# Kernel tuning notes

Measured on AMD Instinct MI355X. Metric: run time of the kernel, lower is better.

## Reference

```python
import jax, jax.numpy as jnp
import numpy as np

C_S, C_Z, C_H = 384, 128, 32
N, L = 4, 384
EPS = 1e-5  # torch LayerNorm default


def setup_inputs() -> dict:
    key = jax.random.key(0)
    ks = jax.random.split(key, 8)
    s = jax.random.normal(ks[0], (N, L, C_S), dtype=jnp.float32)
    ln_g = jnp.ones((C_S,), jnp.float32)
    ln_b = jnp.zeros((C_S,), jnp.float32)
    W1 = jax.random.normal(ks[1], (C_S, C_H), jnp.float32) / np.sqrt(C_S)
    b1 = jax.random.normal(ks[2], (C_H,), jnp.float32) * 0.02
    W2 = jax.random.normal(ks[3], (C_S, C_H), jnp.float32) / np.sqrt(C_S)
    b2 = jax.random.normal(ks[4], (C_H,), jnp.float32) * 0.02
    # linear_out has init='final' (zeros) in training; use random values for a
    # meaningful numerical baseline.
    Wo = jax.random.normal(ks[5], (C_H * C_H, C_Z), jnp.float32) / np.sqrt(C_H * C_H)
    bo = jax.random.normal(ks[6], (C_Z,), jnp.float32) * 0.02
    return {"s": s, "ln_g": ln_g, "ln_b": ln_b, "W1": W1, "b1": b1,
            "W2": W2, "b2": b2, "Wo": Wo, "bo": bo}


def reference(s, ln_g, ln_b, W1, b1, W2, b2, Wo, bo):
    # LayerNorm over c_s
    mu = jnp.mean(s, axis=-1, keepdims=True)
    var = jnp.mean(jnp.square(s - mu), axis=-1, keepdims=True)
    sn = (s - mu) * jax.lax.rsqrt(var + EPS) * ln_g + ln_b
    a = sn @ W1 + b1  # [N, L, c_h]
    b = sn @ W2 + b2  # [N, L, c_h]
    # Original: outer product a[n,i,c]*b[n,j,d] flattened as c*c_h+d, then linear_out.
    # Algebraically fused: never materialize the [N,L,L,c_h^2] tensor.
    Wo3 = Wo.reshape(C_H, C_H, C_Z)  # index order (c, d, z) matches c*c_h+d flattening
    z = jnp.einsum('nic,njd,cdz->nijz', a, b, Wo3, optimize=True) + bo
    return z  # [N, L, L, c_z]
```

## Files before the change

kernel.cpp:

```cpp
#include <hip/hip_runtime.h>
#include <hip/hip_bf16.h>

#define CS 384
#define CH 32
#define CZ 128
#define LL 384
#define NL 1536
#define EPS 1e-5f

typedef float v4f __attribute__((ext_vector_type(4)));
typedef short s8v __attribute__((ext_vector_type(8)));
typedef unsigned short u8s __attribute__((ext_vector_type(8)));

static __device__ __forceinline__ unsigned short f2bf(float x) {
    unsigned int b = __float_as_uint(x);
    b += 0x7FFFu + ((b >> 16) & 1u);
    return (unsigned short)(b >> 16);
}

__global__ __launch_bounds__(256) void k_bf(
    const float* __restrict__ s, const float* __restrict__ g, const float* __restrict__ be,
    const float* __restrict__ W2, const float* __restrict__ pb2,
    unsigned short* __restrict__ BfG)
{
    const int r0 = blockIdx.x * 4;
    const int t  = threadIdx.x;

    __shared__ float sn[4][392];
    __shared__ float part[4][2][32];

    {
        const int w = t >> 6, lane = t & 63;
        const float* srow = s + (size_t)(r0 + w) * CS;
        float x[6];
        #pragma unroll
        for (int k = 0; k < 6; ++k) x[k] = srow[lane + k * 64];
        float p = x[0] + x[1] + x[2] + x[3] + x[4] + x[5];
        #pragma unroll
        for (int m = 1; m < 64; m <<= 1) p += __shfl_xor(p, m);
        const float mu = p * (1.0f / CS);
        float q = 0.f;
        #pragma unroll
        for (int k = 0; k < 6; ++k) { float d = x[k] - mu; q += d * d; }
        #pragma unroll
        for (int m = 1; m < 64; m <<= 1) q += __shfl_xor(q, m);
        const float rstd = rsqrtf(q * (1.0f / CS) + EPS);
        #pragma unroll
        for (int k = 0; k < 6; ++k) {
            const int c = lane + k * 64;
            sn[w][c] = (x[k] - mu) * rstd * g[c] + be[c];
        }
    }
    __syncthreads();

    {
        const int h = t & 31, ch = (t >> 5) & 1, rw = t >> 6;
        const float* snr = sn[rw];
        float acc = 0.f;
        const int c0 = ch * 192;
        #pragma unroll 8
        for (int c = c0; c < c0 + 192; ++c)
            acc += snr[c] * W2[c * CH + h];
        part[rw][ch][h] = acc;
    }
    __syncthreads();

    if (t < 128) {
        const int rw = t >> 5, h = t & 31;
        const float v = part[rw][0][h] + part[rw][1][h] + pb2[h];
        const int row = r0 + rw;
        const int n = row / LL, jr = row % LL;
        const int jt = jr >> 4, l16 = jr & 15;
        BfG[(((size_t)(n * 24 + jt)) * 64 + l16 + 16 * (h >> 3)) * 8 + (h & 7)] = f2bf(v);
    }
}

__global__ __launch_bounds__(256, 3) void k_out_f(
    const float* __restrict__ s, const float* __restrict__ g, const float* __restrict__ be,
    const float* __restrict__ W1, const float* __restrict__ pb1,
    const float* __restrict__ Wo, const unsigned short* __restrict__ BfG,
    const float* __restrict__ bo, float* __restrict__ out)
{
    const int r = blockIdx.x;
    const int t = threadIdx.x;
    const int l = t & 63, w = t >> 6;
    const int g2 = l >> 4, c16 = l & 15;
    const int li = l & 31, hi2 = l >> 5;
    const int n = r / LL;

    __shared__ float sn[392];
    __shared__ float red[8];
    __shared__ float part[8][32];
    __shared__ float Afl[CH];
    __shared__ __align__(16) float Msub[4096];
    __shared__ __align__(16) float bounce[4][2048];

    {
        const float* srow = s + (size_t)r * CS;
        const float e0 = srow[t];
        const float e1 = (t < 128) ? srow[256 + t] : 0.f;
        float p = e0 + e1;
        #pragma unroll
        for (int m = 1; m < 64; m <<= 1) p += __shfl_xor(p, m);
        if (l == 0) red[w] = p;
        __syncthreads();
        const float mu = (red[0] + red[1] + red[2] + red[3]) * (1.0f / CS);
        __syncthreads();
        const float d0 = e0 - mu, d1 = e1 - mu;
        float q = d0 * d0 + ((t < 128) ? d1 * d1 : 0.f);
        #pragma unroll
        for (int m = 1; m < 64; m <<= 1) q += __shfl_xor(q, m);
        if (l == 0) red[w] = q;
        __syncthreads();
        const float var = (red[0] + red[1] + red[2] + red[3]) * (1.0f / CS);
        const float rstd = rsqrtf(var + EPS);
        sn[t] = d0 * rstd * g[t] + be[t];
        if (t < 128) sn[256 + t] = d1 * rstd * g[256 + t] + be[256 + t];
    }
    __syncthreads();

    {
        const int h = t & 31, cs = t >> 5;
        float acc = 0.f;
        const int c0 = cs * 48;
        #pragma unroll 8
        for (int c = c0; c < c0 + 48; ++c)
            acc += sn[c] * W1[c * CH + h];
        part[cs][h] = acc;
    }
    __syncthreads();
    if (t < 32) {
        float a = pb1[t];
        #pragma unroll
        for (int k = 0; k < 8; ++k) a += part[k][t];
        Afl[t] = a;
    }
    __syncthreads();

    {
        const v4f* Wo4 = (const v4f*)Wo;
        #pragma unroll
        for (int it = 0; it < 4; ++it) {
            const int col = t + it * 256;
            v4f acc = (v4f)(0.f);
            #pragma unroll 8
            for (int c = 0; c < CH; ++c)
                acc += Afl[c] * Wo4[(size_t)c * 1024 + col];
            *(v4f*)&Msub[col * 4] = acc;
        }
    }
    __syncthreads();

    s8v mf[8];
    #pragma unroll
    for (int zt = 0; zt < 8; ++zt) {
        u8s o;
        #pragma unroll
        for (int e = 0; e < 8; ++e)
            o[e] = f2bf(Msub[(g2 * 8 + e) * 128 + zt * 16 + c16]);
        mf[zt] = (s8v)o;
    }

    s8v af[6];
    {
        const s8v* Bfn = (const s8v*)(BfG + (size_t)n * 24 * 64 * 8);
        #pragma unroll
        for (int i = 0; i < 6; ++i) af[i] = Bfn[(w + i * 4) * 64 + l];
    }
    v4f bov[8];
    #pragma unroll
    for (int zt = 0; zt < 8; ++zt) bov[zt] = *(const v4f*)(bo + zt * 16 + g2 * 4);

    char* myl = (char*)bounce[w];
    v4f* outv = (v4f*)(out + (size_t)r * LL * CZ);

    #pragma unroll
    for (int i = 0; i < 6; ++i) {
        const int jt = w + i * 4;

        #pragma unroll
        for (int zt = 0; zt < 8; ++zt) {
            v4f d = __builtin_amdgcn_mfma_f32_16x16x32_bf16(mf[zt], af[i], (v4f)(0.f), 0, 0, 0);
            d += bov[zt];
            const int byte = (c16 << 9) + (((zt << 6) + (g2 << 4)) ^ ((c16 & 7) << 4));
            *(v4f*)(myl + byte) = d;
        }
        asm volatile("s_waitcnt lgkmcnt(0)" ::: "memory");

        #pragma unroll
        for (int i2 = 0; i2 < 8; ++i2) {
            const int rw2 = 2 * i2 + hi2;
            const int byte = (rw2 << 9) + (((li << 4)) ^ ((rw2 & 7) << 4));
            const v4f v = *(const v4f*)(myl + byte);
            outv[(size_t)(jt * 16 + rw2) * 32 + li] = v;
        }
    }
}

extern "C" void kernel_launch(void* const* d_in, const int* in_sizes, int n_in,
                              void* d_out, int out_size, void* d_ws, size_t ws_size,
                              hipStream_t stream) {
    const float* s  = (const float*)d_in[0];
    const float* g  = (const float*)d_in[1];
    const float* be = (const float*)d_in[2];
    const float* W1 = (const float*)d_in[3];
    const float* b1 = (const float*)d_in[4];
    const float* W2 = (const float*)d_in[5];
    const float* b2 = (const float*)d_in[6];
    const float* Wo = (const float*)d_in[7];
    const float* bo = (const float*)d_in[8];
    float* out = (float*)d_out;

    if (ws_size < 98304u) return;
    unsigned short* Bf = (unsigned short*)d_ws;

    k_bf   <<<NL / 4, 256, 0, stream>>>(s, g, be, W2, b2, Bf);
    k_out_f<<<NL, 256, 0, stream>>>(s, g, be, W1, b1, Wo, Bf, bo, out);
}
```

Before: 85.55 us.

## Process two rows per block and pre-convert Wo to bf16 once

The first kernel now also converts Wo to bf16 in workspace. The output kernel handles two L rows per block, so each Wo load feeds two A vectors when building the 32x128 M matrices. M is stored directly as transposed bf16 in shared memory, which replaces the strided per-element conversion from fp32. The aim is to halve the per-row Wo traffic and drop redundant conversion work, at the cost of fewer blocks, more shared memory, and an extra barrier between rows.

After: 81.00 us. 1.06x faster.

```diff
diff --git a/kernel.cpp b/kernel.cpp
--- a/kernel.cpp
+++ b/kernel.cpp
@@ -17,14 +17,33 @@
     b += 0x7FFFu + ((b >> 16) & 1u);
     return (unsigned short)(b >> 16);
 }
+static __device__ __forceinline__ v4f bf4_to_f4(ushort4 h) {
+    v4f r;
+    r.x = __uint_as_float((unsigned)h.x << 16);
+    r.y = __uint_as_float((unsigned)h.y << 16);
+    r.z = __uint_as_float((unsigned)h.z << 16);
+    r.w = __uint_as_float((unsigned)h.w << 16);
+    return r;
+}
 
 __global__ __launch_bounds__(256) void k_bf(
     const float* __restrict__ s, const float* __restrict__ g, const float* __restrict__ be,
     const float* __restrict__ W2, const float* __restrict__ pb2,
-    unsigned short* __restrict__ BfG)
+    const float* __restrict__ Wo,
+    unsigned short* __restrict__ BfG, unsigned short* __restrict__ Wob)
 {
     const int r0 = blockIdx.x * 4;
     const int t  = threadIdx.x;
+
+    {
+        const int idx = blockIdx.x * 256 + t;
+        if (idx < (CH * CH * CZ) / 4) {
+            const v4f v = ((const v4f*)Wo)[idx];
+            ushort4 h;
+            h.x = f2bf(v.x); h.y = f2bf(v.y); h.z = f2bf(v.z); h.w = f2bf(v.w);
+            ((ushort4*)Wob)[idx] = h;
+        }
+    }
 
     __shared__ float sn[4][392];
     __shared__ float part[4][2][32];
@@ -78,88 +97,87 @@
 __global__ __launch_bounds__(256, 3) void k_out_f(
     const float* __restrict__ s, const float* __restrict__ g, const float* __restrict__ be,
     const float* __restrict__ W1, const float* __restrict__ pb1,
-    const float* __restrict__ Wo, const unsigned short* __restrict__ BfG,
+    const unsigned short* __restrict__ Wob, const unsigned short* __restrict__ BfG,
     const float* __restrict__ bo, float* __restrict__ out)
 {
-    const int r = blockIdx.x;
-    const int t = threadIdx.x;
+    const int b  = blockIdx.x;
+    const int r0 = b * 2;
+    const int n  = r0 / LL;
+    const int t  = threadIdx.x;
     const int l = t & 63, w = t >> 6;
     const int g2 = l >> 4, c16 = l & 15;
     const int li = l & 31, hi2 = l >> 5;
-    const int n = r / LL;
-
-    __shared__ float sn[392];
-    __shared__ float red[8];
-    __shared__ float part[8][32];
-    __shared__ float Afl[CH];
-    __shared__ __align__(16) float Msub[4096];
-    __shared__ __align__(16) float bounce[4][2048];
-
-    {
-        const float* srow = s + (size_t)r * CS;
-        const float e0 = srow[t];
-        const float e1 = (t < 128) ? srow[256 + t] : 0.f;
-        float p = e0 + e1;
+
+    __shared__ __align__(16) char smem[16384 + 32768];
+    unsigned short* MsubT = (unsigned short*)smem;
+    float (*sn)[392]      = (float(*)[392])(smem + 16384);
+    float (*part)[4][32]  = (float(*)[4][32])(smem + 16384 + 3200);
+    float* Afl            = (float*)(smem + 16384 + 3200 + 1024);
+    char*  bounceBase     = smem + 16384;
+
+    if (w < 2) {
+        const float* srow = s + (size_t)(r0 + w) * CS;
+        float x[6];
+        #pragma unroll
+        for (int k = 0; k < 6; ++k) x[k] = srow[l + k * 64];
+        float p = x[0] + x[1] + x[2] + x[3] + x[4] + x[5];
         #pragma unroll
         for (int m = 1; m < 64; m <<= 1) p += __shfl_xor(p, m);
-        if (l == 0) red[w] = p;
-        __syncthreads();
-        const float mu = (red[0] + red[1] + red[2] + red[3]) * (1.0f / CS);
-        __syncthreads();
-        const float d0 = e0 - mu, d1 = e1 - mu;
-        float q = d0 * d0 + ((t < 128) ? d1 * d1 : 0.f);
+        const float mu = p * (1.0f / CS);
+        float q = 0.f;
+        #pragma unroll
+        for (int k = 0; k < 6; ++k) { float d = x[k] - mu; q += d * d; }
         #pragma unroll
         for (int m = 1; m < 64; m <<= 1) q += __shfl_xor(q, m);
-        if (l == 0) red[w] = q;
-        __syncthreads();
-        const float var = (red[0] + red[1] + red[2] + red[3]) * (1.0f / CS);
-        const float rstd = rsqrtf(var + EPS);
-        sn[t] = d0 * rstd * g[t] + be[t];
-        if (t < 128) sn[256 + t] = d1 * rstd * g[256 + t] + be[256 + t];
-    }
-    __syncthreads();
-
-    {
-        const int h = t & 31, cs = t >> 5;
+        const float rstd = rsqrtf(q * (1.0f / CS) + EPS);
+        #pragma unroll
+        for (int k = 0; k < 6; ++k) {
+            const int c = l + k * 64;
+            sn[w][c] = (x[k] - mu) * rstd * g[c] + be[c];
+        }
+    }
+    __syncthreads();
+
+    {
+        const int h = t & 31, cs = (t >> 5) & 3, rw = t >> 7;
+        const float* snr = sn[rw];
         float acc = 0.f;
-        const int c0 = cs * 48;
+        const int c0 = cs * 96;
         #pragma unroll 8
-        for (int c = c0; c < c0 + 48; ++c)
-            acc += sn[c] * W1[c * CH + h];
-        part[cs][h] = acc;
-    }
-    __syncthreads();
-    if (t < 32) {
-        float a = pb1[t];
-        #pragma unroll
-        for (int k = 0; k < 8; ++k) a += part[k][t];
-        Afl[t] = a;
-    }
-    __syncthreads();
-
-    {
-        const v4f* Wo4 = (const v4f*)Wo;
+        for (int c = c0; c < c0 + 96; ++c)
+            acc += snr[c] * W1[c * CH + h];
+        part[rw][cs][h] = acc;
+    }
+    __syncthreads();
+    if (t < 64) {
+        const int rw = t >> 5, h = t & 31;
+        Afl[rw * 32 + h] = part[rw][0][h] + part[rw][1][h] + part[rw][2][h]
+                         + part[rw][3][h] + pb1[h];
+    }
+    __syncthreads();
+
+    {
+        const ushort4* Wo4 = (const ushort4*)Wob;
         #pragma unroll
         for (int it = 0; it < 4; ++it) {
             const int col = t + it * 256;
-            v4f acc = (v4f)(0.f);
+            const int d = col >> 5, zq = col & 31;
+            v4f a0 = (v4f)(0.f), a1 = (v4f)(0.f);
             #pragma unroll 8
-            for (int c = 0; c < CH; ++c)
-                acc += Afl[c] * Wo4[(size_t)c * 1024 + col];
-            *(v4f*)&Msub[col * 4] = acc;
-        }
-    }
-    __syncthreads();
-
-    s8v mf[8];
-    #pragma unroll
-    for (int zt = 0; zt < 8; ++zt) {
-        u8s o;
-        #pragma unroll
-        for (int e = 0; e < 8; ++e)
-            o[e] = f2bf(Msub[(g2 * 8 + e) * 128 + zt * 16 + c16]);
-        mf[zt] = (s8v)o;
-    }
+            for (int c = 0; c < CH; ++c) {
+                const v4f wv = bf4_to_f4(Wo4[(size_t)c * 1024 + col]);
+                a0 += Afl[c] * wv;
+                a1 += Afl[32 + c] * wv;
+            }
+            #pragma unroll
+            for (int j = 0; j < 4; ++j) {
+                const int z = zq * 4 + j;
+                MsubT[z * 32 + d]        = f2bf(a0[j]);
+                MsubT[4096 + z * 32 + d] = f2bf(a1[j]);
+            }
+        }
+    }
+    __syncthreads();
 
     s8v af[6];
     {
@@ -171,29 +189,42 @@
     #pragma unroll
     for (int zt = 0; zt < 8; ++zt) bov[zt] = *(const v4f*)(bo + zt * 16 + g2 * 4);
 
-    char* myl = (char*)bounce[w];
-    v4f* outv = (v4f*)(out + (size_t)r * LL * CZ);
+    char* myl = bounceBase + w * 8192;
 
     #pragma unroll
-    for (int i = 0; i < 6; ++i) {
-        const int jt = w + i * 4;
-
-        #pragma unroll
-        for (int zt = 0; zt < 8; ++zt) {
-            v4f d = __builtin_amdgcn_mfma_f32_16x16x32_bf16(mf[zt], af[i], (v4f)(0.f), 0, 0, 0);
-            d += bov[zt];
-            const int byte = (c16 << 9) + (((zt << 6) + (g2 << 4)) ^ ((c16 & 7) << 4));
-            *(v4f*)(myl + byte) = d;
-        }
-        asm volatile("s_waitcnt lgkmcnt(0)" ::: "memory");
-
-        #pragma unroll
-        for (int i2 = 0; i2 < 8; ++i2) {
-            const int rw2 = 2 * i2 + hi2;
-            const int byte = (rw2 << 9) + (((li << 4)) ^ ((rw2 & 7) << 4));
-            const v4f v = *(const v4f*)(myl + byte);
-            outv[(size_t)(jt * 16 + rw2) * 32 + li] = v;
-        }
+    for (int rr = 0; rr < 2; ++rr) {
+        s8v mf[8];
+        {
+            const unsigned short* Ms = MsubT + rr * 4096;
+            #pragma unroll
+            for (int zt = 0; zt < 8; ++zt)
+                mf[zt] = *(const s8v*)(Ms + (zt * 16 + c16) * 32 + g2 * 8);
+        }
+
+        v4f* outv = (v4f*)(out + (size_t)(r0 + rr) * LL * CZ);
+
+        #pragma unroll
+        for (int i = 0; i < 6; ++i) {
+            const int jt = w + i * 4;
+
+            #pragma unroll
+            for (int zt = 0; zt < 8; ++zt) {
+                v4f d = __builtin_amdgcn_mfma_f32_16x16x32_bf16(mf[zt], af[i], (v4f)(0.f), 0, 0, 0);
+                d += bov[zt];
+                const int byte = (c16 << 9) + (((zt << 6) + (g2 << 4)) ^ ((c16 & 7) << 4));
+                *(v4f*)(myl + byte) = d;
+            }
+            asm volatile("s_waitcnt lgkmcnt(0)" ::: "memory");
+
+            #pragma unroll
+            for (int i2 = 0; i2 < 8; ++i2) {
+                const int rw2 = 2 * i2 + hi2;
+                const int byte = (rw2 << 9) + (((li << 4)) ^ ((rw2 & 7) << 4));
+                const v4f v = *(const v4f*)(myl + byte);
+                outv[(size_t)(jt * 16 + rw2) * 32 + li] = v;
+            }
+        }
+        __syncthreads();
     }
 }
 
@@ -211,9 +242,10 @@
     const float* bo = (const float*)d_in[8];
     float* out = (float*)d_out;
 
-    if (ws_size < 98304u) return;
-    unsigned short* Bf = (unsigned short*)d_ws;
-
-    k_bf   <<<NL / 4, 256, 0, stream>>>(s, g, be, W2, b2, Bf);
-    k_out_f<<<NL, 256, 0, stream>>>(s, g, be, W1, b1, Wo, Bf, bo, out);
-}
+    if (ws_size < 98304u + 262144u) return;
+    unsigned short* Bf  = (unsigned short*)d_ws;
+    unsigned short* Wob = (unsigned short*)((char*)d_ws + 98304);
+
+    k_bf   <<<NL / 4, 256, 0, stream>>>(s, g, be, W2, b2, Wo, Bf, Wob);
+    k_out_f<<<NL / 2, 256, 0, stream>>>(s, g, be, W1, b1, Wob, Bf, bo, out);
+}
```

## Pre-convert Wo to bf16, store Msub transposed bf16, overlay shared memory

Applied to the files above, without the earlier changes.

The first kernel now also converts Wo to bf16 in workspace, so each output block reads half as many bytes of Wo when forming its per-row Msub matrix. Msub is written directly as a swizzled, transposed bf16 tile, which lets the MFMA A-fragments be loaded with single vector reads instead of eight scalar loads plus conversions. The layernorm scratch and bounce buffers share one overlaid LDS region, shrinking shared memory per block and possibly allowing more blocks per CU. In exchange, Wo is rounded to bf16 before the Msub product, adding error, and the workspace requirement grows.

Result: no change. 84.25 us (-1.5%).

```diff
diff --git a/kernel.cpp b/kernel.cpp
--- a/kernel.cpp
+++ b/kernel.cpp
@@ -17,14 +17,33 @@
     b += 0x7FFFu + ((b >> 16) & 1u);
     return (unsigned short)(b >> 16);
 }
+static __device__ __forceinline__ v4f bf4_to_f4(ushort4 h) {
+    v4f r;
+    r.x = __uint_as_float((unsigned)h.x << 16);
+    r.y = __uint_as_float((unsigned)h.y << 16);
+    r.z = __uint_as_float((unsigned)h.z << 16);
+    r.w = __uint_as_float((unsigned)h.w << 16);
+    return r;
+}
 
 __global__ __launch_bounds__(256) void k_bf(
     const float* __restrict__ s, const float* __restrict__ g, const float* __restrict__ be,
     const float* __restrict__ W2, const float* __restrict__ pb2,
-    unsigned short* __restrict__ BfG)
+    const float* __restrict__ Wo,
+    unsigned short* __restrict__ BfG, unsigned short* __restrict__ Wob)
 {
     const int r0 = blockIdx.x * 4;
     const int t  = threadIdx.x;
+
+    {
+        const int idx = blockIdx.x * 256 + t;
+        if (idx < (CH * CH * CZ) / 4) {
+            const v4f v = ((const v4f*)Wo)[idx];
+            ushort4 h;
+            h.x = f2bf(v.x); h.y = f2bf(v.y); h.z = f2bf(v.z); h.w = f2bf(v.w);
+            ((ushort4*)Wob)[idx] = h;
+        }
+    }
 
     __shared__ float sn[4][392];
     __shared__ float part[4][2][32];
@@ -78,22 +97,24 @@
 __global__ __launch_bounds__(256, 3) void k_out_f(
     const float* __restrict__ s, const float* __restrict__ g, const float* __restrict__ be,
     const float* __restrict__ W1, const float* __restrict__ pb1,
-    const float* __restrict__ Wo, const unsigned short* __restrict__ BfG,
+    const unsigned short* __restrict__ Wob, const unsigned short* __restrict__ BfG,
     const float* __restrict__ bo, float* __restrict__ out)
 {
     const int r = blockIdx.x;
+    const int n = r / LL;
     const int t = threadIdx.x;
     const int l = t & 63, w = t >> 6;
     const int g2 = l >> 4, c16 = l & 15;
     const int li = l & 31, hi2 = l >> 5;
-    const int n = r / LL;
-
-    __shared__ float sn[392];
-    __shared__ float red[8];
-    __shared__ float part[8][32];
-    __shared__ float Afl[CH];
-    __shared__ __align__(16) float Msub[4096];
-    __shared__ __align__(16) float bounce[4][2048];
+
+    __shared__ __align__(16) char smem[8192 + 32768];
+    unsigned short* MsubT = (unsigned short*)smem;
+    char* ovl = smem + 8192;
+    float* sn   = (float*)ovl;
+    float* red  = (float*)(ovl + 1568);
+    float (*part)[32] = (float(*)[32])(ovl + 1600);
+    float* Afl  = (float*)(ovl + 2624);
+    char*  bounceBase = ovl;
 
     {
         const float* srow = s + (size_t)r * CS;
@@ -138,27 +159,29 @@
     __syncthreads();
 
     {
-        const v4f* Wo4 = (const v4f*)Wo;
+        const ushort4* Wo4 = (const ushort4*)Wob;
         #pragma unroll
         for (int it = 0; it < 4; ++it) {
             const int col = t + it * 256;
-            v4f acc = (v4f)(0.f);
+            const int d = col >> 5, zq = col & 31;
+            v4f a0 = (v4f)(0.f);
             #pragma unroll 8
             for (int c = 0; c < CH; ++c)
-                acc += Afl[c] * Wo4[(size_t)c * 1024 + col];
-            *(v4f*)&Msub[col * 4] = acc;
+                a0 += Afl[c] * bf4_to_f4(Wo4[(size_t)c * 1024 + col]);
+            const int bsw = ((d >> 3) ^ (zq & 3)) * 8 + (d & 7);
+            #pragma unroll
+            for (int j = 0; j < 4; ++j)
+                MsubT[(zq * 4 + j) * 32 + bsw] = f2bf(a0[j]);
         }
     }
     __syncthreads();
 
     s8v mf[8];
-    #pragma unroll
-    for (int zt = 0; zt < 8; ++zt) {
-        u8s o;
-        #pragma unroll
-        for (int e = 0; e < 8; ++e)
-            o[e] = f2bf(Msub[(g2 * 8 + e) * 128 + zt * 16 + c16]);
-        mf[zt] = (s8v)o;
+    {
+        const int rblk = (g2 ^ ((c16 >> 2) & 3)) * 8;
+        #pragma unroll
+        for (int zt = 0; zt < 8; ++zt)
+            mf[zt] = *(const s8v*)(MsubT + (zt * 16 + c16) * 32 + rblk);
     }
 
     s8v af[6];
@@ -171,7 +194,7 @@
     #pragma unroll
     for (int zt = 0; zt < 8; ++zt) bov[zt] = *(const v4f*)(bo + zt * 16 + g2 * 4);
 
-    char* myl = (char*)bounce[w];
+    char* myl = bounceBase + w * 8192;
     v4f* outv = (v4f*)(out + (size_t)r * LL * CZ);
 
     #pragma unroll
@@ -211,9 +234,10 @@
     const float* bo = (const float*)d_in[8];
     float* out = (float*)d_out;
 
-    if (ws_size < 98304u) return;
-    unsigned short* Bf = (unsigned short*)d_ws;
-
-    k_bf   <<<NL / 4, 256, 0, stream>>>(s, g, be, W2, b2, Bf);
-    k_out_f<<<NL, 256, 0, stream>>>(s, g, be, W1, b1, Wo, Bf, bo, out);
-}
+    if (ws_size < 98304u + 262144u) return;
+    unsigned short* Bf  = (unsigned short*)d_ws;
+    unsigned short* Wob = (unsigned short*)((char*)d_ws + 98304);
+
+    k_bf   <<<NL / 4, 256, 0, stream>>>(s, g, be, W2, b2, Wo, Bf, Wob);
+    k_out_f<<<NL, 256, 0, stream>>>(s, g, be, W1, b1, Wob, Bf, bo, out);
+}
```
